# Performance work log

Hardware: AMD Instinct MI355X
Metric: run time of the kernel (lower is better)

Reference implementation:

```python
import jax, jax.numpy as jnp
import numpy as np

N = 50000   # nodes
E = 600000  # edges (both relations mixed)
D = 128     # in_features == out_features


def _gcn(x, W, b, row, col, w, n):
    """PyG GCNConv: add self-loops (weight 1), symmetric normalization, linear, aggregate, bias.
    Edges with w==0 contribute nothing to degree or messages (== masked subgraph)."""
    idx = jnp.arange(n)
    srow = jnp.concatenate([row, idx])
    scol = jnp.concatenate([col, idx])
    sw = jnp.concatenate([w, jnp.ones((n,), x.dtype)])
    deg = jax.ops.segment_sum(sw, scol, num_segments=n)                 # [n]
    dinv = jnp.where(deg > 0, jax.lax.rsqrt(jnp.maximum(deg, 1e-12)), 0.0)
    norm = dinv[srow] * sw * dinv[scol]                                 # [E+n]
    h = x @ W                                                           # [n, D]
    out = jax.ops.segment_sum(h[srow] * norm[:, None], scol, num_segments=n)
    return out + b


def setup_inputs() -> dict:
    key = jax.random.key(0)
    ks = jax.random.split(key, 12)
    s_in = 1.0 / np.sqrt(D)
    s_g = 1.0 / np.sqrt(3 * D)
    return {
        "x": jax.random.normal(ks[0], (N, D), dtype=jnp.float32),
        "edge_index": jax.random.randint(ks[1], (2, E), 0, N, dtype=jnp.int64),
        "edge_type": jax.random.randint(ks[2], (E,), 0, 2, dtype=jnp.int64),
        "W_sl": jax.random.normal(ks[3], (D, D), dtype=jnp.float32) * s_in,
        "b_sl": jnp.zeros((D,), jnp.float32),
        "W0": jax.random.normal(ks[4], (D, D), dtype=jnp.float32) * s_in,
        "b0": jnp.zeros((D,), jnp.float32),
        "W1": jax.random.normal(ks[5], (D, D), dtype=jnp.float32) * s_in,
        "b1": jnp.zeros((D,), jnp.float32),
        "W_g": jax.random.normal(ks[6], (3 * D, D), dtype=jnp.float32) * s_g,
        "b_g": jnp.zeros((D,), jnp.float32),
    }


def reference(x, edge_index, edge_type, W_sl, b_sl, W0, b0, W1, b1, W_g, b_g):
    n = x.shape[0]
    row, col = edge_index[0], edge_index[1]
    x_x = x @ W_sl + b_sl                                   # self-loop linear
    w0 = (edge_type == 0).astype(x.dtype)
    w1 = (edge_type == 1).astype(x.dtype)
    x_n = _gcn(x, W0, b0, row, col, w0, n)                  # relation 0 GCN
    x_d = _gcn(x, W1, b1, row, col, w1, n)                  # relation 1 GCN
    gat_raw = jax.nn.softmax(jnp.concatenate([x_x, x_n, x_d], axis=1) @ W_g + b_g, axis=-1)
    gat = jnp.cumsum(gat_raw, axis=-1)                      # ordered-neuron gate
    return x_d[:, ::-1] * gat + x_x + x_n
```

## Files before the change

kernel.cpp:

```cpp
#include <hip/hip_runtime.h>
#include <hip/hip_bf16.h>
#include <hip/hip_fp16.h>
#include <math.h>


typedef __attribute__((ext_vector_type(8))) short bf16x8;
typedef __attribute__((ext_vector_type(4))) float f32x4;
typedef __attribute__((ext_vector_type(8))) unsigned short ushort8;

__device__ inline float b2f(unsigned short u) {
  return __uint_as_float(((unsigned)u) << 16);
}
__device__ inline unsigned short f2bf(float f) {
  __hip_bfloat16 b = __float2bfloat16(f);
  return *reinterpret_cast<unsigned short*>(&b);
}

__global__ __launch_bounds__(256) void pack_count(const float* __restrict__ Wsl,
                                                  const float* __restrict__ W0,
                                                  const float* __restrict__ W1,
                                                  const float* __restrict__ Wg,
                                                  unsigned short* __restrict__ Wp3,
                                                  unsigned short* __restrict__ Wgp,
                                                  const int* __restrict__ col,
                                                  const int* __restrict__ etype,
                                                  int* __restrict__ deg,
                                                  int* __restrict__ erank, int E, int n) {
  if (blockIdx.x < 48) {
    int tid = blockIdx.x * 256 + threadIdx.x;
    if (tid < 6144) {
      int z = tid / 2048, r = tid % 2048;
      int lane = r & 63, idx = r >> 6;
      int kf = idx & 3, ct = idx >> 2;
      const float* W = (z == 0) ? Wsl : (z == 1) ? W0 : W1;
      unsigned short* dst = Wp3 + (size_t)z * 16384 + (size_t)r * 8;
      int krow = kf * 32 + (lane >> 4) * 8;
      int ccol = ct * 16 + (lane & 15);
#pragma unroll
      for (int j = 0; j < 8; ++j) dst[j] = f2bf(W[(size_t)(krow + j) * 128 + ccol]);
    } else {
      int r = tid - 6144;
      int lane = r & 63, idx = r >> 6;
      int kf = idx % 12, ct = idx / 12;
      unsigned short* dst = Wgp + (size_t)r * 8;
      int krow = kf * 32 + (lane >> 4) * 8;
      int ccol = ct * 16 + (lane & 15);
#pragma unroll
      for (int j = 0; j < 8; ++j) dst[j] = f2bf(Wg[(size_t)(krow + j) * 128 + ccol]);
    }
  } else {
    int e = (blockIdx.x - 48) * 256 + threadIdx.x;
    if (e >= E) return;
    int rk = atomicAdd(&deg[(size_t)etype[e] * n + col[e]], 1);
    erank[e] = rk;
  }
}

__global__ __launch_bounds__(256) void dinv_scan1(const int* __restrict__ deg,
                                                  float* __restrict__ dinv,
                                                  int* __restrict__ partials,
                                                  int n2, int nb) {
  int tid = threadIdx.x;
  if ((int)blockIdx.x < nb) {
    int base = blockIdx.x * 2048 + tid * 8;
    int s = 0;
#pragma unroll
    for (int k = 0; k < 8; ++k) {
      int i = base + k;
      if (i < n2) s += deg[i];
    }
    __shared__ int sb[256];
    sb[tid] = s;
    __syncthreads();
    for (int o = 128; o; o >>= 1) {
      if (tid < o) sb[tid] += sb[tid + o];
      __syncthreads();
    }
    if (tid == 0) partials[blockIdx.x] = sb[0];
  } else {
    int i = (blockIdx.x - nb) * 256 + tid;
    if (i < n2) dinv[i] = rsqrtf((float)deg[i] + 1.0f);
  }
}

__global__ __launch_bounds__(256) void scan3b(const int* __restrict__ partials,
                                              const int* __restrict__ deg,
                                              int* __restrict__ row_start, int n2, int nb) {
  __shared__ int sb[256];
  __shared__ int ex[256];
  int tid = threadIdx.x;
  int pv = (tid < nb) ? partials[tid] : 0;
  sb[tid] = pv;
  __syncthreads();
  for (int o = 1; o < 256; o <<= 1) {
    int t = (tid >= o) ? sb[tid - o] : 0;
    __syncthreads();
    sb[tid] += t;
    __syncthreads();
  }
  ex[tid] = sb[tid] - pv;
  __syncthreads();
  int base = ex[blockIdx.x];
  __syncthreads();

  int bstart = blockIdx.x * 2048 + tid * 8;
  int v[8];
  int s = 0;
#pragma unroll
  for (int k = 0; k < 8; ++k) {
    int i = bstart + k;
    v[k] = (i < n2) ? deg[i] : 0;
    s += v[k];
  }
  sb[tid] = s;
  __syncthreads();
  for (int o = 1; o < 256; o <<= 1) {
    int t = (tid >= o) ? sb[tid - o] : 0;
    __syncthreads();
    sb[tid] += t;
    __syncthreads();
  }
  int run = base + (sb[tid] - s);
#pragma unroll
  for (int k = 0; k < 8; ++k) {
    int i = bstart + k;
    if (i < n2) {
      row_start[i] = run;
      run += v[k];
    }
  }
}

__global__ __launch_bounds__(256) void gemm3_fill(
    const float* __restrict__ x, const unsigned short* __restrict__ Wp3,
    const float* __restrict__ bsl, unsigned short* __restrict__ hx,
    unsigned short* __restrict__ h0, unsigned short* __restrict__ h1,
    const int* __restrict__ row, const int* __restrict__ col,
    const int* __restrict__ etype, const int* __restrict__ erank,
    const int* __restrict__ row_start, const float* __restrict__ dinv,
    unsigned int* __restrict__ ebuf, int n, int E, int gb) {
  __shared__ unsigned short xs[64 * 136];
  int tid = threadIdx.x;
  if ((int)blockIdx.x >= gb) {
    int e = (blockIdx.x - gb) * 256 + tid;
    if (e >= E) return;
    int r = row[e], c = col[e], t = etype[e];
    int b = t * n + c;
    float nrm = dinv[t * n + r] * dinv[b];
    int pos = row_start[b] + erank[e];
    unsigned int rec = (unsigned int)(r & 0xFFFF) |
                       ((unsigned int)__half_as_ushort(__float2half_rn(nrm)) << 16);
    ebuf[pos] = rec;
    return;
  }
  int row0 = blockIdx.x * 64;
  {
    const float4* xg = (const float4*)(x + (size_t)row0 * 128);
    int maxv = (n - row0) * 32;
#pragma unroll
    for (int i = 0; i < 8; ++i) {
      int idx = tid + i * 256;
      float4 v = {0.f, 0.f, 0.f, 0.f};
      if (idx < maxv) v = xg[idx];
      int rr = idx >> 5, c4 = idx & 31;
      ushort4 u;
      u.x = f2bf(v.x);
      u.y = f2bf(v.y);
      u.z = f2bf(v.z);
      u.w = f2bf(v.w);
      *(ushort4*)&xs[rr * 136 + c4 * 4] = u;
    }
  }
  __syncthreads();
  int w = tid >> 6;
  int l = tid & 63;
  int q = l >> 4;
  int c = l & 15;
  bf16x8 af[4];
#pragma unroll
  for (int kf = 0; kf < 4; ++kf)
    af[kf] = *(const bf16x8*)&xs[(w * 16 + c) * 136 + kf * 32 + q * 8];

  int gr0 = row0 + w * 16 + q * 4;
#pragma unroll
  for (int z = 0; z < 3; ++z) {
    const bf16x8* Bp = (const bf16x8*)(Wp3 + (size_t)z * 16384);
    unsigned short* h = (z == 0) ? hx : (z == 1) ? h0 : h1;
#pragma unroll
    for (int ct = 0; ct < 8; ++ct) {
      f32x4 acc = {0.f, 0.f, 0.f, 0.f};
#pragma unroll
      for (int kf = 0; kf < 4; ++kf)
        acc = __builtin_amdgcn_mfma_f32_16x16x32_bf16(af[kf], Bp[(ct * 4 + kf) * 64 + l], acc, 0, 0, 0);
      int fc = ct * 16 + c;
      float bias = (z == 0) ? bsl[fc] : 0.f;
#pragma unroll
      for (int i = 0; i < 4; ++i) {
        int gr = gr0 + i;
        if (gr < n) h[(size_t)gr * 128 + fc] = f2bf(acc[i] + bias);
      }
    }
  }
}

__global__ __launch_bounds__(256) void gather2(const unsigned short* __restrict__ h0,
                                               const unsigned short* __restrict__ h1,
                                               const unsigned int* __restrict__ ebuf,
                                               const int* __restrict__ row_start,
                                               const int* __restrict__ deg,
                                               const float* __restrict__ dinv,
                                               const float* __restrict__ b0,
                                               const float* __restrict__ b1,
                                               unsigned short* __restrict__ xn,
                                               unsigned short* __restrict__ xd, int n) {
  int t = blockIdx.y;
  long long gid = (long long)blockIdx.x * 256 + threadIdx.x;
  int node = (int)(gid >> 3);
  if (node >= n) return;
  int sub = (int)(gid & 7);
  const ushort8* hp8 = (const ushort8*)(t ? h1 : h0);
  const float* bias = t ? b1 : b0;
  unsigned short* out = t ? xd : xn;
  const int* rs = row_start + (size_t)t * n;
  const int* dg = deg + (size_t)t * n;
  float di = dinv[(size_t)t * n + node];

  float accA[8], accB[8];
  float acc2A[8] = {0, 0, 0, 0, 0, 0, 0, 0}, acc2B[8] = {0, 0, 0, 0, 0, 0, 0, 0};
  {
    ushort8 sa = hp8[(size_t)node * 16 + sub * 2];
    ushort8 sbv = hp8[(size_t)node * 16 + sub * 2 + 1];
    float sl = di * di;
#pragma unroll
    for (int k = 0; k < 8; ++k) {
      accA[k] = fmaf(b2f(sa[k]), sl, bias[sub * 16 + k]);
      accB[k] = fmaf(b2f(sbv[k]), sl, bias[sub * 16 + 8 + k]);
    }
  }
  int s = rs[node];
  int e = s + dg[node];
  int j = s;
  for (; j + 1 < e; j += 2) {
    unsigned int r0 = ebuf[j], r1 = ebuf[j + 1];
    int i0 = (int)(r0 & 0xFFFFu), i1 = (int)(r1 & 0xFFFFu);
    float n0 = __half2float(__ushort_as_half((unsigned short)(r0 >> 16)));
    float n1 = __half2float(__ushort_as_half((unsigned short)(r1 >> 16)));
    ushort8 v0a = hp8[(size_t)i0 * 16 + sub * 2];
    ushort8 v0b = hp8[(size_t)i0 * 16 + sub * 2 + 1];
    ushort8 v1a = hp8[(size_t)i1 * 16 + sub * 2];
    ushort8 v1b = hp8[(size_t)i1 * 16 + sub * 2 + 1];
#pragma unroll
    for (int k = 0; k < 8; ++k) {
      accA[k] = fmaf(b2f(v0a[k]), n0, accA[k]);
      accB[k] = fmaf(b2f(v0b[k]), n0, accB[k]);
      acc2A[k] = fmaf(b2f(v1a[k]), n1, acc2A[k]);
      acc2B[k] = fmaf(b2f(v1b[k]), n1, acc2B[k]);
    }
  }
  if (j < e) {
    unsigned int r0 = ebuf[j];
    int i0 = (int)(r0 & 0xFFFFu);
    float n0 = __half2float(__ushort_as_half((unsigned short)(r0 >> 16)));
    ushort8 v0a = hp8[(size_t)i0 * 16 + sub * 2];
    ushort8 v0b = hp8[(size_t)i0 * 16 + sub * 2 + 1];
#pragma unroll
    for (int k = 0; k < 8; ++k) {
      accA[k] = fmaf(b2f(v0a[k]), n0, accA[k]);
      accB[k] = fmaf(b2f(v0b[k]), n0, accB[k]);
    }
  }
  ushort8 ua, ub;
#pragma unroll
  for (int k = 0; k < 8; ++k) {
    ua[k] = f2bf(accA[k] + acc2A[k]);
    ub[k] = f2bf(accB[k] + acc2B[k]);
  }
  ((ushort8*)out)[(size_t)node * 16 + sub * 2] = ua;
  ((ushort8*)out)[(size_t)node * 16 + sub * 2 + 1] = ub;
}

__global__ __launch_bounds__(64) void gate_combine(const unsigned short* __restrict__ hx,
                                                   const unsigned short* __restrict__ xn,
                                                   const unsigned short* __restrict__ xd,
                                                   const unsigned short* __restrict__ Wgp,
                                                   const float* __restrict__ bg,
                                                   float* __restrict__ out, int n) {
  int row0 = blockIdx.x * 16;
  int l = threadIdx.x;
  int q = l >> 4;
  int c = l & 15;
  int ar = row0 + c;
  if (ar >= n) ar = n - 1;
  bf16x8 af[12];
  {
    const unsigned short* p0 = hx + (size_t)ar * 128 + q * 8;
    const unsigned short* p1 = xn + (size_t)ar * 128 + q * 8;
    const unsigned short* p2 = xd + (size_t)ar * 128 + q * 8;
#pragma unroll
    for (int k = 0; k < 4; ++k) {
      af[k] = *(const bf16x8*)(p0 + k * 32);
      af[4 + k] = *(const bf16x8*)(p1 + k * 32);
      af[8 + k] = *(const bf16x8*)(p2 + k * 32);
    }
  }
  const bf16x8* Bp = (const bf16x8*)Wgp;
  f32x4 acc[8];
#pragma unroll
  for (int ct = 0; ct < 8; ++ct) acc[ct] = (f32x4){0.f, 0.f, 0.f, 0.f};
#pragma unroll
  for (int kf = 0; kf < 12; ++kf) {
    bf16x8 a = af[kf];
#pragma unroll
    for (int ct = 0; ct < 8; ++ct)
      acc[ct] = __builtin_amdgcn_mfma_f32_16x16x32_bf16(a, Bp[(ct * 12 + kf) * 64 + l], acc[ct], 0, 0, 0);
  }
#pragma unroll
  for (int ct = 0; ct < 8; ++ct) {
    float bgv = bg[ct * 16 + c];
#pragma unroll
    for (int i = 0; i < 4; ++i) acc[ct][i] += bgv;
  }
#pragma unroll
  for (int i = 0; i < 4; ++i) {
    float m = acc[0][i];
#pragma unroll
    for (int ct = 1; ct < 8; ++ct) m = fmaxf(m, acc[ct][i]);
#pragma unroll
    for (int o = 1; o < 16; o <<= 1) m = fmaxf(m, __shfl_xor(m, o));
    float e[8];
    float s = 0.f;
#pragma unroll
    for (int ct = 0; ct < 8; ++ct) {
      e[ct] = __expf(acc[ct][i] - m);
      s += e[ct];
    }
#pragma unroll
    for (int o = 1; o < 16; o <<= 1) s += __shfl_xor(s, o);
    float inv = 1.0f / s;
    int gr = row0 + q * 4 + i;
    float run = 0.f;
#pragma unroll
    for (int ct = 0; ct < 8; ++ct) {
      float p = e[ct];
#pragma unroll
      for (int o = 1; o < 16; o <<= 1) {
        float t = __shfl_up(p, o);
        if (c >= o) p += t;
      }
      float T = __shfl(p, q * 16 + 15);
      float gat = (run + p) * inv;
      run += T;
      int f = ct * 16 + c;
      if (gr < n) {
        size_t gb = (size_t)gr * 128;
        float xxv = b2f(hx[gb + f]);
        float xnv = b2f(xn[gb + f]);
        float xdv = b2f(xd[gb + 127 - f]);
        out[gb + f] = fmaf(xdv, gat, xxv + xnv);
      }
    }
  }
}

extern "C" void kernel_launch(void* const* d_in, const int* in_sizes, int n_in,
                              void* d_out, int out_size, void* d_ws, size_t ws_size,
                              hipStream_t stream) {
  const float* x = (const float*)d_in[0];
  const int* eidx = (const int*)d_in[1];
  const int* etype = (const int*)d_in[2];
  const float* Wsl = (const float*)d_in[3];
  const float* bsl = (const float*)d_in[4];
  const float* W0 = (const float*)d_in[5];
  const float* b0 = (const float*)d_in[6];
  const float* W1 = (const float*)d_in[7];
  const float* b1 = (const float*)d_in[8];
  const float* Wg = (const float*)d_in[9];
  const float* bg = (const float*)d_in[10];
  int n = in_sizes[0] / 128;
  int E = in_sizes[2];
  const int* row = eidx;
  const int* col = eidx + E;
  int n2 = 2 * n;

  char* w = (char*)d_ws;
  int* deg = (int*)w;             w += (size_t)n2 * 4;
  float* dinv = (float*)w;        w += (size_t)n2 * 4;
  int* row_start = (int*)w;       w += (size_t)n2 * 4;
  int* partials = (int*)w;        w += 1024;
  unsigned int* ebuf = (unsigned int*)w;  w += (size_t)E * 4;
  int* erank = (int*)w;           w += (size_t)E * 4;
  unsigned short* Wp3 = (unsigned short*)w;  w += 3 * 128 * 128 * 2;
  unsigned short* Wgp = (unsigned short*)w;  w += 384 * 128 * 2;
  unsigned short* hx = (unsigned short*)w;   w += (size_t)n * 128 * 2;
  unsigned short* h0 = (unsigned short*)w;   w += (size_t)n * 128 * 2;
  unsigned short* h1 = (unsigned short*)w;   w += (size_t)n * 128 * 2;
  unsigned short* xn = (unsigned short*)w;   w += (size_t)n * 128 * 2;
  unsigned short* xd = (unsigned short*)w;
  float* out = (float*)d_out;

  hipMemsetAsync(deg, 0, (size_t)n2 * 4, stream);

  int cd_blocks = (E + 255) / 256;
  pack_count<<<48 + cd_blocks, 256, 0, stream>>>(Wsl, W0, W1, Wg, Wp3, Wgp,
                                                 col, etype, deg, erank, E, n);
  int nb = (n2 + 2047) / 2048;
  dinv_scan1<<<nb + (n2 + 255) / 256, 256, 0, stream>>>(deg, dinv, partials, n2, nb);
  scan3b<<<nb, 256, 0, stream>>>(partials, deg, row_start, n2, nb);

  int gemm_blocks = (n + 63) / 64;
  gemm3_fill<<<gemm_blocks + cd_blocks, 256, 0, stream>>>(
      x, Wp3, bsl, hx, h0, h1, row, col, etype, erank, row_start, dinv, ebuf,
      n, E, gemm_blocks);

  int ga_blocks = (int)(((long long)n * 8 + 255) / 256);
  gather2<<<dim3(ga_blocks, 2), 256, 0, stream>>>(h0, h1, ebuf, row_start, deg, dinv,
                                                  b0, b1, xn, xd, n);
  gate_combine<<<(n + 15) / 16, 64, 0, stream>>>(hx, xn, xd, Wgp, bg, out, n);
}
```

Measured before the change: 145.7 us.

## Fuse neighbor gather with gate GEMM via shared memory; stage GEMM stores

Merges the two-relation gather kernel and the gate/combine kernel into one kernel. Each 128-thread block aggregates 32 nodes per relation into shared memory, then runs the gate MFMA and the combine step from LDS, so the xn/xd intermediates are never written to or reread from global memory. The GEMM kernel now writes its output tiles through LDS so rows go out as coalesced 16-byte stores instead of scattered 2-byte stores. In exchange, each gather wave loops serially over four nodes, which lowers parallelism for the latency-bound gather, and the GEMM gains extra barriers.

Result: slower. 156.3 us (+7.3%).

```diff
diff --git a/kernel.cpp b/kernel.cpp
--- a/kernel.cpp
+++ b/kernel.cpp
@@ -180,8 +180,8 @@
 #pragma unroll
   for (int kf = 0; kf < 4; ++kf)
     af[kf] = *(const bf16x8*)&xs[(w * 16 + c) * 136 + kf * 32 + q * 8];
-
-  int gr0 = row0 + w * 16 + q * 4;
+  __syncthreads();
+
 #pragma unroll
   for (int z = 0; z < 3; ++z) {
     const bf16x8* Bp = (const bf16x8*)(Wp3 + (size_t)z * 16384);
@@ -195,113 +195,123 @@
       int fc = ct * 16 + c;
       float bias = (z == 0) ? bsl[fc] : 0.f;
 #pragma unroll
-      for (int i = 0; i < 4; ++i) {
-        int gr = gr0 + i;
-        if (gr < n) h[(size_t)gr * 128 + fc] = f2bf(acc[i] + bias);
-      }
-    }
-  }
-}
-
-__global__ __launch_bounds__(256) void gather2(const unsigned short* __restrict__ h0,
-                                               const unsigned short* __restrict__ h1,
-                                               const unsigned int* __restrict__ ebuf,
-                                               const int* __restrict__ row_start,
-                                               const int* __restrict__ deg,
-                                               const float* __restrict__ dinv,
-                                               const float* __restrict__ b0,
-                                               const float* __restrict__ b1,
-                                               unsigned short* __restrict__ xn,
-                                               unsigned short* __restrict__ xd, int n) {
-  int t = blockIdx.y;
-  long long gid = (long long)blockIdx.x * 256 + threadIdx.x;
-  int node = (int)(gid >> 3);
-  if (node >= n) return;
-  int sub = (int)(gid & 7);
-  const ushort8* hp8 = (const ushort8*)(t ? h1 : h0);
-  const float* bias = t ? b1 : b0;
-  unsigned short* out = t ? xd : xn;
-  const int* rs = row_start + (size_t)t * n;
-  const int* dg = deg + (size_t)t * n;
-  float di = dinv[(size_t)t * n + node];
-
-  float accA[8], accB[8];
-  float acc2A[8] = {0, 0, 0, 0, 0, 0, 0, 0}, acc2B[8] = {0, 0, 0, 0, 0, 0, 0, 0};
+      for (int i = 0; i < 4; ++i)
+        xs[(w * 16 + q * 4 + i) * 136 + fc] = f2bf(acc[i] + bias);
+    }
+    __syncthreads();
+#pragma unroll
+    for (int i = 0; i < 4; ++i) {
+      int idx = tid + i * 256;
+      int rr = idx >> 4, c8 = idx & 15;
+      int gr = row0 + rr;
+      if (gr < n)
+        *(ushort8*)(h + (size_t)gr * 128 + c8 * 8) = *(const ushort8*)&xs[rr * 136 + c8 * 8];
+    }
+    __syncthreads();
+  }
+}
+
+__global__ __launch_bounds__(128) void gather_gate(
+    const unsigned short* __restrict__ hx, const unsigned short* __restrict__ h0,
+    const unsigned short* __restrict__ h1, const unsigned int* __restrict__ ebuf,
+    const int* __restrict__ row_start, const int* __restrict__ deg,
+    const float* __restrict__ dinv, const float* __restrict__ b0,
+    const float* __restrict__ b1, const unsigned short* __restrict__ Wgp,
+    const float* __restrict__ bg, float* __restrict__ out, int n) {
+  __shared__ unsigned short xs[3][32][136];
+  int tid = threadIdx.x;
+  int wv = tid >> 6;
+  int l = tid & 63;
+  int node0 = blockIdx.x * 32;
+
+#pragma unroll
+  for (int i = 0; i < 4; ++i) {
+    int idx = tid + i * 128;
+    int rr = idx >> 4, c8 = idx & 15;
+    int gr = node0 + rr;
+    if (gr > n - 1) gr = n - 1;
+    *(ushort8*)&xs[0][rr][c8 * 8] = *(const ushort8*)(hx + (size_t)gr * 128 + c8 * 8);
+  }
+
   {
-    ushort8 sa = hp8[(size_t)node * 16 + sub * 2];
-    ushort8 sbv = hp8[(size_t)node * 16 + sub * 2 + 1];
-    float sl = di * di;
-#pragma unroll
-    for (int k = 0; k < 8; ++k) {
-      accA[k] = fmaf(b2f(sa[k]), sl, bias[sub * 16 + k]);
-      accB[k] = fmaf(b2f(sbv[k]), sl, bias[sub * 16 + 8 + k]);
-    }
-  }
-  int s = rs[node];
-  int e = s + dg[node];
-  int j = s;
-  for (; j + 1 < e; j += 2) {
-    unsigned int r0 = ebuf[j], r1 = ebuf[j + 1];
-    int i0 = (int)(r0 & 0xFFFFu), i1 = (int)(r1 & 0xFFFFu);
-    float n0 = __half2float(__ushort_as_half((unsigned short)(r0 >> 16)));
-    float n1 = __half2float(__ushort_as_half((unsigned short)(r1 >> 16)));
-    ushort8 v0a = hp8[(size_t)i0 * 16 + sub * 2];
-    ushort8 v0b = hp8[(size_t)i0 * 16 + sub * 2 + 1];
-    ushort8 v1a = hp8[(size_t)i1 * 16 + sub * 2];
-    ushort8 v1b = hp8[(size_t)i1 * 16 + sub * 2 + 1];
-#pragma unroll
-    for (int k = 0; k < 8; ++k) {
-      accA[k] = fmaf(b2f(v0a[k]), n0, accA[k]);
-      accB[k] = fmaf(b2f(v0b[k]), n0, accB[k]);
-      acc2A[k] = fmaf(b2f(v1a[k]), n1, acc2A[k]);
-      acc2B[k] = fmaf(b2f(v1b[k]), n1, acc2B[k]);
-    }
-  }
-  if (j < e) {
-    unsigned int r0 = ebuf[j];
-    int i0 = (int)(r0 & 0xFFFFu);
-    float n0 = __half2float(__ushort_as_half((unsigned short)(r0 >> 16)));
-    ushort8 v0a = hp8[(size_t)i0 * 16 + sub * 2];
-    ushort8 v0b = hp8[(size_t)i0 * 16 + sub * 2 + 1];
-#pragma unroll
-    for (int k = 0; k < 8; ++k) {
-      accA[k] = fmaf(b2f(v0a[k]), n0, accA[k]);
-      accB[k] = fmaf(b2f(v0b[k]), n0, accB[k]);
-    }
-  }
-  ushort8 ua, ub;
-#pragma unroll
-  for (int k = 0; k < 8; ++k) {
-    ua[k] = f2bf(accA[k] + acc2A[k]);
-    ub[k] = f2bf(accB[k] + acc2B[k]);
-  }
-  ((ushort8*)out)[(size_t)node * 16 + sub * 2] = ua;
-  ((ushort8*)out)[(size_t)node * 16 + sub * 2 + 1] = ub;
-}
-
-__global__ __launch_bounds__(64) void gate_combine(const unsigned short* __restrict__ hx,
-                                                   const unsigned short* __restrict__ xn,
-                                                   const unsigned short* __restrict__ xd,
-                                                   const unsigned short* __restrict__ Wgp,
-                                                   const float* __restrict__ bg,
-                                                   float* __restrict__ out, int n) {
-  int row0 = blockIdx.x * 16;
-  int l = threadIdx.x;
+    int t = wv;
+    const ushort8* hp8 = (const ushort8*)(t ? h1 : h0);
+    const float* bias = t ? b1 : b0;
+    const int* rs = row_start + (size_t)t * n;
+    const int* dg = deg + (size_t)t * n;
+    const float* dv = dinv + (size_t)t * n;
+    int sub = l & 7;
+#pragma unroll
+    for (int p = 0; p < 4; ++p) {
+      int rr = p * 8 + (l >> 3);
+      int node = node0 + rr;
+      if (node > n - 1) node = n - 1;
+      float di = dv[node];
+      float accA[8], accB[8];
+      float acc2A[8] = {0, 0, 0, 0, 0, 0, 0, 0}, acc2B[8] = {0, 0, 0, 0, 0, 0, 0, 0};
+      {
+        ushort8 sa = hp8[(size_t)node * 16 + sub * 2];
+        ushort8 sbv = hp8[(size_t)node * 16 + sub * 2 + 1];
+        float sl = di * di;
+#pragma unroll
+        for (int k = 0; k < 8; ++k) {
+          accA[k] = fmaf(b2f(sa[k]), sl, bias[sub * 16 + k]);
+          accB[k] = fmaf(b2f(sbv[k]), sl, bias[sub * 16 + 8 + k]);
+        }
+      }
+      int s = rs[node];
+      int e = s + dg[node];
+      int j = s;
+      for (; j + 1 < e; j += 2) {
+        unsigned int r0 = ebuf[j], r1 = ebuf[j + 1];
+        int i0 = (int)(r0 & 0xFFFFu), i1 = (int)(r1 & 0xFFFFu);
+        float n0 = __half2float(__ushort_as_half((unsigned short)(r0 >> 16)));
+        float n1 = __half2float(__ushort_as_half((unsigned short)(r1 >> 16)));
+        ushort8 v0a = hp8[(size_t)i0 * 16 + sub * 2];
+        ushort8 v0b = hp8[(size_t)i0 * 16 + sub * 2 + 1];
+        ushort8 v1a = hp8[(size_t)i1 * 16 + sub * 2];
+        ushort8 v1b = hp8[(size_t)i1 * 16 + sub * 2 + 1];
+#pragma unroll
+        for (int k = 0; k < 8; ++k) {
+          accA[k] = fmaf(b2f(v0a[k]), n0, accA[k]);
+          accB[k] = fmaf(b2f(v0b[k]), n0, accB[k]);
+          acc2A[k] = fmaf(b2f(v1a[k]), n1, acc2A[k]);
+          acc2B[k] = fmaf(b2f(v1b[k]), n1, acc2B[k]);
+        }
+      }
+      if (j < e) {
+        unsigned int r0 = ebuf[j];
+        int i0 = (int)(r0 & 0xFFFFu);
+        float n0 = __half2float(__ushort_as_half((unsigned short)(r0 >> 16)));
+        ushort8 v0a = hp8[(size_t)i0 * 16 + sub * 2];
+        ushort8 v0b = hp8[(size_t)i0 * 16 + sub * 2 + 1];
+#pragma unroll
+        for (int k = 0; k < 8; ++k) {
+          accA[k] = fmaf(b2f(v0a[k]), n0, accA[k]);
+          accB[k] = fmaf(b2f(v0b[k]), n0, accB[k]);
+        }
+      }
+      ushort8 ua, ub;
+#pragma unroll
+      for (int k = 0; k < 8; ++k) {
+        ua[k] = f2bf(accA[k] + acc2A[k]);
+        ub[k] = f2bf(accB[k] + acc2B[k]);
+      }
+      *(ushort8*)&xs[1 + t][rr][sub * 16] = ua;
+      *(ushort8*)&xs[1 + t][rr][sub * 16 + 8] = ub;
+    }
+  }
+  __syncthreads();
+
   int q = l >> 4;
   int c = l & 15;
-  int ar = row0 + c;
-  if (ar >= n) ar = n - 1;
+  int rbase = wv * 16;
   bf16x8 af[12];
-  {
-    const unsigned short* p0 = hx + (size_t)ar * 128 + q * 8;
-    const unsigned short* p1 = xn + (size_t)ar * 128 + q * 8;
-    const unsigned short* p2 = xd + (size_t)ar * 128 + q * 8;
-#pragma unroll
-    for (int k = 0; k < 4; ++k) {
-      af[k] = *(const bf16x8*)(p0 + k * 32);
-      af[4 + k] = *(const bf16x8*)(p1 + k * 32);
-      af[8 + k] = *(const bf16x8*)(p2 + k * 32);
-    }
+#pragma unroll
+  for (int k = 0; k < 4; ++k) {
+    af[k] = *(const bf16x8*)&xs[0][rbase + c][k * 32 + q * 8];
+    af[4 + k] = *(const bf16x8*)&xs[1][rbase + c][k * 32 + q * 8];
+    af[8 + k] = *(const bf16x8*)&xs[2][rbase + c][k * 32 + q * 8];
   }
   const bf16x8* Bp = (const bf16x8*)Wgp;
   f32x4 acc[8];
@@ -337,7 +347,8 @@
 #pragma unroll
     for (int o = 1; o < 16; o <<= 1) s += __shfl_xor(s, o);
     float inv = 1.0f / s;
-    int gr = row0 + q * 4 + i;
+    int rr = rbase + q * 4 + i;
+    int gr = node0 + rr;
     float run = 0.f;
 #pragma unroll
     for (int ct = 0; ct < 8; ++ct) {
@@ -352,11 +363,10 @@
       run += T;
       int f = ct * 16 + c;
       if (gr < n) {
-        size_t gb = (size_t)gr * 128;
-        float xxv = b2f(hx[gb + f]);
-        float xnv = b2f(xn[gb + f]);
-        float xdv = b2f(xd[gb + 127 - f]);
-        out[gb + f] = fmaf(xdv, gat, xxv + xnv);
+        float xxv = b2f(xs[0][rr][f]);
+        float xnv = b2f(xs[1][rr][f]);
+        float xdv = b2f(xs[2][rr][127 - f]);
+        out[(size_t)gr * 128 + f] = fmaf(xdv, gat, xxv + xnv);
       }
     }
   }
@@ -393,9 +403,7 @@
   unsigned short* Wgp = (unsigned short*)w;  w += 384 * 128 * 2;
   unsigned short* hx = (unsigned short*)w;   w += (size_t)n * 128 * 2;
   unsigned short* h0 = (unsigned short*)w;   w += (size_t)n * 128 * 2;
-  unsigned short* h1 = (unsigned short*)w;   w += (size_t)n * 128 * 2;
-  unsigned short* xn = (unsigned short*)w;   w += (size_t)n * 128 * 2;
-  unsigned short* xd = (unsigned short*)w;
+  unsigned short* h1 = (unsigned short*)w;
   float* out = (float*)d_out;
 
   hipMemsetAsync(deg, 0, (size_t)n2 * 4, stream);
@@ -412,8 +420,6 @@
       x, Wp3, bsl, hx, h0, h1, row, col, etype, erank, row_start, dinv, ebuf,
       n, E, gemm_blocks);
 
-  int ga_blocks = (int)(((long long)n * 8 + 255) / 256);
-  gather2<<<dim3(ga_blocks, 2), 256, 0, stream>>>(h0, h1, ebuf, row_start, deg, dinv,
-                                                  b0, b1, xn, xd, n);
-  gate_combine<<<(n + 15) / 16, 64, 0, stream>>>(hx, xn, xd, Wgp, bg, out, n);
-}
+  gather_gate<<<(n + 31) / 32, 128, 0, stream>>>(hx, h0, h1, ebuf, row_start, deg,
+                                                 dinv, b0, b1, Wgp, bg, out, n);
+}
```

## Stage GEMM outputs through LDS and share gate weights across waves

Applied to the files above, without the earlier changes.

In gemm3_fill, the MFMA results are first written into the shared-memory tile. They are then stored to global memory as full 16-byte row vectors, replacing the scattered 2-byte stores. gate_combine now runs 4 waves per block (64 rows) and cooperatively double-buffers the gate weight fragments in LDS, so each wave no longer reads the whole W_g from global/L2. This adds extra __syncthreads, and the larger block may lower scheduling flexibility for the tail rows.

New measurement: 146.3 us. Within noise of the previous version (+0.4%).

```diff
diff --git a/kernel.cpp b/kernel.cpp
--- a/kernel.cpp
+++ b/kernel.cpp
@@ -180,8 +180,8 @@
 #pragma unroll
   for (int kf = 0; kf < 4; ++kf)
     af[kf] = *(const bf16x8*)&xs[(w * 16 + c) * 136 + kf * 32 + q * 8];
-
-  int gr0 = row0 + w * 16 + q * 4;
+  __syncthreads();
+
 #pragma unroll
   for (int z = 0; z < 3; ++z) {
     const bf16x8* Bp = (const bf16x8*)(Wp3 + (size_t)z * 16384);
@@ -195,11 +195,19 @@
       int fc = ct * 16 + c;
       float bias = (z == 0) ? bsl[fc] : 0.f;
 #pragma unroll
-      for (int i = 0; i < 4; ++i) {
-        int gr = gr0 + i;
-        if (gr < n) h[(size_t)gr * 128 + fc] = f2bf(acc[i] + bias);
-      }
-    }
+      for (int i = 0; i < 4; ++i)
+        xs[(w * 16 + q * 4 + i) * 136 + fc] = f2bf(acc[i] + bias);
+    }
+    __syncthreads();
+#pragma unroll
+    for (int i = 0; i < 4; ++i) {
+      int idx = tid + i * 256;
+      int rr = idx >> 4, c8 = idx & 15;
+      int gr = row0 + rr;
+      if (gr < n)
+        *(ushort8*)(h + (size_t)gr * 128 + c8 * 8) = *(const ushort8*)&xs[rr * 136 + c8 * 8];
+    }
+    __syncthreads();
   }
 }
 
@@ -279,18 +287,19 @@
   ((ushort8*)out)[(size_t)node * 16 + sub * 2 + 1] = ub;
 }
 
-__global__ __launch_bounds__(64) void gate_combine(const unsigned short* __restrict__ hx,
-                                                   const unsigned short* __restrict__ xn,
-                                                   const unsigned short* __restrict__ xd,
-                                                   const unsigned short* __restrict__ Wgp,
-                                                   const float* __restrict__ bg,
-                                                   float* __restrict__ out, int n) {
-  int row0 = blockIdx.x * 16;
-  int l = threadIdx.x;
+__global__ __launch_bounds__(256) void gate_combine(
+    const unsigned short* __restrict__ hx, const unsigned short* __restrict__ xn,
+    const unsigned short* __restrict__ xd, const unsigned short* __restrict__ Wgp,
+    const float* __restrict__ bg, float* __restrict__ out, int n) {
+  __shared__ __align__(16) unsigned short Bs[2][8 * 64 * 8];
+  int tid = threadIdx.x;
+  int wv = tid >> 6;
+  int l = tid & 63;
   int q = l >> 4;
   int c = l & 15;
+  int row0 = blockIdx.x * 64 + wv * 16;
   int ar = row0 + c;
-  if (ar >= n) ar = n - 1;
+  if (ar > n - 1) ar = n - 1;
   bf16x8 af[12];
   {
     const unsigned short* p0 = hx + (size_t)ar * 128 + q * 8;
@@ -303,16 +312,36 @@
       af[8 + k] = *(const bf16x8*)(p2 + k * 32);
     }
   }
-  const bf16x8* Bp = (const bf16x8*)Wgp;
+  {
+    int u = tid;
+#pragma unroll
+    for (int r = 0; r < 2; ++r, u += 256) {
+      int ct = u >> 6, ll = u & 63;
+      *(ushort8*)&Bs[0][u * 8] = *(const ushort8*)(Wgp + ((size_t)(ct * 12) * 64 + ll) * 8);
+    }
+  }
+  __syncthreads();
   f32x4 acc[8];
 #pragma unroll
   for (int ct = 0; ct < 8; ++ct) acc[ct] = (f32x4){0.f, 0.f, 0.f, 0.f};
 #pragma unroll
   for (int kf = 0; kf < 12; ++kf) {
+    int cur = kf & 1;
+    if (kf < 11) {
+      int u = tid;
+#pragma unroll
+      for (int r = 0; r < 2; ++r, u += 256) {
+        int ct = u >> 6, ll = u & 63;
+        *(ushort8*)&Bs[cur ^ 1][u * 8] =
+            *(const ushort8*)(Wgp + ((size_t)(ct * 12 + kf + 1) * 64 + ll) * 8);
+      }
+    }
     bf16x8 a = af[kf];
 #pragma unroll
     for (int ct = 0; ct < 8; ++ct)
-      acc[ct] = __builtin_amdgcn_mfma_f32_16x16x32_bf16(a, Bp[(ct * 12 + kf) * 64 + l], acc[ct], 0, 0, 0);
+      acc[ct] = __builtin_amdgcn_mfma_f32_16x16x32_bf16(
+          a, *(const bf16x8*)&Bs[cur][(ct * 64 + l) * 8], acc[ct], 0, 0, 0);
+    if (kf < 11) __syncthreads();
   }
 #pragma unroll
   for (int ct = 0; ct < 8; ++ct) {
@@ -415,5 +444,5 @@
   int ga_blocks = (int)(((long long)n * 8 + 255) / 256);
   gather2<<<dim3(ga_blocks, 2), 256, 0, stream>>>(h0, h1, ebuf, row_start, deg, dinv,
                                                   b0, b1, xn, xd, n);
-  gate_combine<<<(n + 15) / 16, 64, 0, stream>>>(hx, xn, xd, Wgp, bg, out, n);
-}
+  gate_combine<<<(n + 63) / 64, 256, 0, stream>>>(hx, xn, xd, Wgp, bg, out, n);
+}
```
